# Kernel tuning notes

Hardware: AMD Instinct MI355X
Metric: run time of the kernel (lower is better)

## Reference

```python
import jax, jax.numpy as jnp
import numpy as np

NUM_ENTITIES = 100000
BATCH_SIZE = 4096
E_STATIC = 250000
E_NEW = 4096
D_ENT = 128
D_REL = 64
N_REL = 9
N_TYPES = 3
N_INTENTS = 8
NUM_LAYERS = 3
SCALE = 0.05


def _make_edges(key, n):
    ks = jax.random.split(key, 5)
    src = jax.random.randint(ks[0], (n,), 0, NUM_ENTITIES, dtype=jnp.int32)
    st = jax.random.randint(ks[1], (n,), 0, N_TYPES, dtype=jnp.int32)
    tgt = jax.random.randint(ks[2], (n,), 0, NUM_ENTITIES, dtype=jnp.int32)
    tt = jax.random.randint(ks[3], (n,), 0, N_TYPES, dtype=jnp.int32)
    rel = jax.random.randint(ks[4], (n,), 0, N_REL, dtype=jnp.int32)
    return jnp.stack([src, st, tgt, tt, rel], axis=1)


def setup_inputs() -> dict:
    key = jax.random.key(0)
    ks = jax.random.split(key, 16)
    return {
        'new_edges': _make_edges(ks[0], E_NEW),
        'new_node_types': jax.random.randint(ks[1], (BATCH_SIZE,), 0, N_TYPES, dtype=jnp.int32),
        'static_edges': _make_edges(ks[2], E_STATIC),
        'entity_embeddings': SCALE * jax.random.normal(ks[3], (NUM_ENTITIES - BATCH_SIZE, D_ENT), jnp.float32),
        'default_emb': SCALE * jax.random.normal(ks[4], (N_TYPES, D_ENT), jnp.float32),
        'relation_emb': SCALE * jax.random.normal(ks[5], (N_REL, D_REL), jnp.float32),
        'W_rel': SCALE * jax.random.normal(ks[6], (N_REL, D_ENT, D_REL), jnp.float32),
        'b_rel': SCALE * jax.random.normal(ks[7], (N_REL, D_REL), jnp.float32),
        'W_msg': SCALE * jax.random.normal(ks[8], (N_REL, D_ENT, D_ENT), jnp.float32),
        'W_intent': SCALE * jax.random.normal(ks[9], (N_TYPES, D_ENT, N_INTENTS), jnp.float32),
        'b_intent': SCALE * jax.random.normal(ks[10], (N_TYPES, N_INTENTS), jnp.float32),
        'W_ibn': SCALE * jax.random.normal(ks[11], (N_TYPES, N_INTENTS, N_REL), jnp.float32),
        'b_ibn': SCALE * jax.random.normal(ks[12], (N_TYPES, N_REL), jnp.float32),
    }


def multi_dense(lookups, values, W, b=None, act=None):
    # Same math as tf.gather(W, lookups) followed by values @ w, but computed
    # against all D (<=9) weight slices then selected, to avoid materializing
    # a [E, d_in, d_out] gathered-weights tensor.
    out_all = jnp.einsum('ei,dio->edo', values, W)  # [E, D, d_out]
    out = jnp.take_along_axis(out_all, lookups[:, None, None], axis=1)[:, 0]
    if b is not None:
        out = out + b[lookups]
    return act(out) if act is not None else out


def reference(new_edges, new_node_types, static_edges, entity_embeddings,
              default_emb, relation_emb, W_rel, b_rel, W_msg,
              W_intent, b_intent, W_ibn, b_ibn):
    edges = jnp.concatenate([new_edges, static_edges], axis=0)  # [E, 5]
    sources = edges[:, 0]
    targets = edges[:, 2]
    target_types = edges[:, 3]
    relations = edges[:, 4]

    rel_e = relation_emb[relations]  # [E, D_REL]
    # first BATCH_SIZE entity slots come from type default embeddings
    ent = jnp.concatenate([default_emb[new_node_types], entity_embeddings], axis=0)  # [N, D_ENT]

    layer_edge_weights = []
    for _ in range(NUM_LAYERS):
        src = ent[sources]  # [E, D_ENT]
        tgt = ent[targets]  # [E, D_ENT]
        # per-target intent distribution and per-relation intent weights
        intents = multi_dense(target_types, tgt, W_intent, b_intent, jax.nn.softmax)  # [E, N_INTENTS]
        rel_w = multi_dense(target_types, intents, W_ibn, b_ibn, jax.nn.softmax)  # [E, N_REL]
        iw = jnp.take_along_axis(rel_w, relations[:, None], axis=1)[:, 0]  # [E]
        # per-relation transform of source embeddings
        src_rel = multi_dense(relations, src, W_rel, b_rel, jax.nn.selu)  # [E, D_REL]
        scores = jnp.einsum('er,er,e->e', src_rel, rel_e, iw)  # [E]
        exp_s = jnp.exp(scores)
        denom = jax.ops.segment_sum(exp_s, targets, num_segments=NUM_ENTITIES)  # [N]
        # tf.math.reciprocal_no_nan semantics
        safe = jnp.where(denom != 0, denom, 1.0)
        recip = jnp.where(denom != 0, 1.0 / safe, 0.0)
        dist = exp_s * recip[targets]  # scatter-softmax over incoming edges
        # inference: dropout is identity
        msg = dist[:, None] * multi_dense(relations, src, W_msg, None, None)  # [E, D_ENT]
        ent = jax.ops.segment_sum(msg, targets, num_segments=NUM_ENTITIES)  # [N, D_ENT]
        layer_edge_weights.append(dist)

    return ent, jnp.stack(layer_edge_weights)  # [N, D_ENT], [L, E]
```

## Files before the change

### kernel.cpp

```cpp
#include <hip/hip_runtime.h>
#include <cstddef>
#include <cstdint>

#define NE 100000
#define EN 4096
#define ET 254096
#define D 128
#define DR 64
#define NR 9
#define NT 3
#define NI 8
#define TE 256
#define TILES_X 28

using frag  = __attribute__((ext_vector_type(8))) short;
using f32x4 = __attribute__((ext_vector_type(4))) float;

__device__ __forceinline__ ushort f2b(float x) {
  union { float f; uint32_t u; } v; v.f = x;
  uint32_t r = v.u + 0x7FFFu + ((v.u >> 16) & 1u);
  return (ushort)(r >> 16);
}

__device__ __forceinline__ uint32_t cvtpk(float lo, float hi) {
  uint32_t r;
  asm("v_cvt_pk_bf16_f32 %0, %1, %2" : "=v"(r) : "v"(lo), "v"(hi));
  return r;
}

__device__ __forceinline__ frag lds_rd(const ushort* b, int row, int k) {
  const int ch = ((k >> 3) ^ (row & 7));
  return *(const frag*)(b + row * D + (ch << 3));
}
__device__ __forceinline__ void lds_wr(ushort* b, int row, int ch, frag v) {
  *(frag*)(b + row * D + ((ch ^ (row & 7)) << 3)) = v;
}
__device__ __forceinline__ void lds_wr2(ushort* b, int row, int k, uint32_t v) {
  const int ch = (k >> 3) ^ (row & 7);
  *(uint32_t*)(b + row * D + (ch << 3) + (k & 7)) = v;
}

__global__ void fill_zero(float4* __restrict__ p, int n4) {
  int i = blockIdx.x * blockDim.x + threadIdx.x;
  if (i < n4) p[i] = make_float4(0.f, 0.f, 0.f, 0.f);
}

__global__ void k_init(ushort* __restrict__ entb, const int* __restrict__ ntypes,
                       const float* __restrict__ def, const float* __restrict__ emb) {
  int i = blockIdx.x * blockDim.x + threadIdx.x;
  if (i >= NE * (D / 4)) return;
  int row = i >> 5, ch = i & 31;
  float4 v;
  if (row < EN) v = ((const float4*)(def + ntypes[row] * D))[ch];
  else v = ((const float4*)(emb + (size_t)(row - EN) * D))[ch];
  ushort4 h;
  h.x = f2b(v.x); h.y = f2b(v.y); h.z = f2b(v.z); h.w = f2b(v.w);
  ((ushort4*)entb)[i] = h;
}

__global__ void k_zero_cnt(int* cnt) { if (threadIdx.x < 48) cnt[threadIdx.x] = 0; }

__global__ __launch_bounds__(256) void k_hist(const int* __restrict__ nedg,
                                              const int* __restrict__ sedg,
                                              int* __restrict__ cnt) {
  __shared__ int h[NR];
  if (threadIdx.x < NR) h[threadIdx.x] = 0;
  __syncthreads();
  int e = blockIdx.x * 256 + threadIdx.x;
  if (e < ET) {
    const int* p = (e < EN) ? nedg + (size_t)e * 5 : sedg + (size_t)(e - EN) * 5;
    atomicAdd(&h[p[4]], 1);
  }
  __syncthreads();
  if (threadIdx.x < NR && h[threadIdx.x]) atomicAdd(&cnt[threadIdx.x], h[threadIdx.x]);
}

__global__ void k_prefix(const int* __restrict__ cnt, int* __restrict__ base,
                         int* __restrict__ head) {
  if (threadIdx.x == 0) {
    int acc = 0;
    for (int r = 0; r < NR; r++) { base[r] = acc; head[r] = acc; acc += cnt[r]; }
  }
}

__global__ __launch_bounds__(256) void k_scatter2(const int* __restrict__ nedg,
                                                  const int* __restrict__ sedg,
                                                  int* __restrict__ head,
                                                  int* __restrict__ bucket) {
  __shared__ int h[NR], bb[NR];
  if (threadIdx.x < NR) h[threadIdx.x] = 0;
  __syncthreads();
  int e = blockIdx.x * 256 + threadIdx.x;
  int r = -1, pos = 0;
  if (e < ET) {
    const int* p = (e < EN) ? nedg + (size_t)e * 5 : sedg + (size_t)(e - EN) * 5;
    r = p[4];
    pos = atomicAdd(&h[r], 1);
  }
  __syncthreads();
  if (threadIdx.x < NR)
    bb[threadIdx.x] = h[threadIdx.x] ? atomicAdd(&head[threadIdx.x], h[threadIdx.x]) : 0;
  __syncthreads();
  if (r >= 0) bucket[bb[r] + pos] = e;
}

__global__ __launch_bounds__(256) void k_thist(const int* __restrict__ nedg,
                                               const int* __restrict__ sedg,
                                               int* __restrict__ thist) {
  int e = blockIdx.x * 256 + threadIdx.x;
  if (e >= ET) return;
  const int* p = (e < EN) ? nedg + (size_t)e * 5 : sedg + (size_t)(e - EN) * 5;
  atomicAdd(&thist[p[2]], 1);
}

__global__ __launch_bounds__(256) void k_scan1(const int* __restrict__ hist,
                                               int* __restrict__ local_ex,
                                               int* __restrict__ bsum, int n) {
  __shared__ int s[256];
  int i = blockIdx.x * 256 + threadIdx.x;
  int v = (i < n) ? hist[i] : 0;
  s[threadIdx.x] = v;
  __syncthreads();
  for (int off = 1; off < 256; off <<= 1) {
    int t = (threadIdx.x >= off) ? s[threadIdx.x - off] : 0;
    __syncthreads();
    s[threadIdx.x] += t;
    __syncthreads();
  }
  if (i < n) local_ex[i] = s[threadIdx.x] - v;
  if (threadIdx.x == 255) bsum[blockIdx.x] = s[255];
}

__global__ __launch_bounds__(512) void k_scan2(int* __restrict__ bsum, int nb) {
  __shared__ int s[512];
  int v = (threadIdx.x < nb) ? bsum[threadIdx.x] : 0;
  s[threadIdx.x] = v;
  __syncthreads();
  for (int off = 1; off < 512; off <<= 1) {
    int t = (threadIdx.x >= off) ? s[threadIdx.x - off] : 0;
    __syncthreads();
    s[threadIdx.x] += t;
    __syncthreads();
  }
  if (threadIdx.x < nb) bsum[threadIdx.x] = s[threadIdx.x] - v;
}

__global__ void k_scan3(int* __restrict__ tgt_off, const int* __restrict__ bsum,
                        int* __restrict__ thead) {
  int i = blockIdx.x * 256 + threadIdx.x;
  if (i < NE) {
    int v = tgt_off[i] + bsum[i >> 8];
    tgt_off[i] = v;
    thead[i] = v;
  }
  if (i == 0) tgt_off[NE] = ET;
}

__global__ __launch_bounds__(256) void k_tscatter(const int* __restrict__ nedg,
                                                  const int* __restrict__ sedg,
                                                  int* __restrict__ thead,
                                                  int* __restrict__ tpos,
                                                  int* __restrict__ esorted) {
  int e = blockIdx.x * 256 + threadIdx.x;
  if (e >= ET) return;
  const int* p = (e < EN) ? nedg + (size_t)e * 5 : sedg + (size_t)(e - EN) * 5;
  int pos = atomicAdd(&thead[p[2]], 1);
  tpos[e] = pos;
  esorted[pos] = e;
}

__global__ __launch_bounds__(256) void k_iw(
    const ushort* __restrict__ entb,
    const float* __restrict__ W_int, const float* __restrict__ b_int,
    const float* __restrict__ W_ibn, const float* __restrict__ b_ibn,
    float* __restrict__ IW) {
  __shared__ ushort sE[TE * D];
  __shared__ ushort sWi[NT * 16 * D];
  __shared__ float sInt3[TE * 25];
  __shared__ float sbint[NT * NI], sWibn[NT * NI * NR], sbibn[NT * NR];

  const int tid = threadIdx.x;
  const int lane = tid & 63, wv = tid >> 6, g = lane >> 4, c = lane & 15;

  for (int i = tid; i < NT * NI * (D / 2); i += 256) {
    int tt = i / (NI * D / 2), rem = i % (NI * D / 2), j = rem / (D / 2), k2 = rem % (D / 2);
    const float* Wi = W_int + (size_t)tt * D * NI;
    lds_wr2(sWi, tt * 16 + j, 2 * k2, cvtpk(Wi[(2 * k2) * NI + j], Wi[(2 * k2 + 1) * NI + j]));
  }
  for (int i = tid; i < NT * 8 * (D / 2); i += 256) {
    int tt = i / (8 * D / 2), rem = i % (8 * D / 2), j = rem / (D / 2), k2 = rem % (D / 2);
    lds_wr2(sWi, tt * 16 + 8 + j, 2 * k2, 0u);
  }
  for (int i = tid; i < NT * NI; i += 256) sbint[i] = b_int[i];
  for (int i = tid; i < NT * NI * NR; i += 256) sWibn[i] = W_ibn[i];
  for (int i = tid; i < NT * NR; i += 256) sbibn[i] = b_ibn[i];

  const int ebase = blockIdx.x * TE;
  for (int i = tid; i < TE * 16; i += 256) {
    int row = i >> 4, ch = i & 15;
    int ent = ebase + row;
    frag v = {};
    if (ent < NE) v = ((const frag*)(entb + (size_t)ent * D))[ch];
    lds_wr(sE, row, ch, v);
  }
  __syncthreads();

  f32x4 accI[4][NT];
#pragma unroll
  for (int mt = 0; mt < 4; mt++)
#pragma unroll
    for (int tt = 0; tt < NT; tt++) accI[mt][tt] = (f32x4){0.f, 0.f, 0.f, 0.f};
#pragma unroll
  for (int ks = 0; ks < 4; ks++) {
    const int k = ks * 32 + g * 8;
    frag b[NT];
#pragma unroll
    for (int tt = 0; tt < NT; tt++) b[tt] = lds_rd(sWi, tt * 16 + c, k);
#pragma unroll
    for (int mt = 0; mt < 4; mt++) {
      frag a = lds_rd(sE, (wv * 4 + mt) * 16 + c, k);
#pragma unroll
      for (int tt = 0; tt < NT; tt++)
        accI[mt][tt] = __builtin_amdgcn_mfma_f32_16x16x32_bf16(a, b[tt], accI[mt][tt], 0, 0, 0);
    }
  }
  if (c < NI) {
#pragma unroll
    for (int mt = 0; mt < 4; mt++) {
      const int rb = (wv * 4 + mt) * 16 + g * 4;
#pragma unroll
      for (int tt = 0; tt < NT; tt++)
#pragma unroll
        for (int q = 0; q < 4; q++) sInt3[(rb + q) * 25 + tt * 8 + c] = accI[mt][tt][q];
    }
  }
  __syncthreads();

  const int ent = ebase + tid;
  if (ent < NE) {
    float* outp = IW + (size_t)ent * NT * NR;
#pragma unroll
    for (int tt = 0; tt < NT; tt++) {
      float it[NI], mx = -1e30f;
#pragma unroll
      for (int j = 0; j < NI; j++) {
        it[j] = sInt3[tid * 25 + tt * 8 + j] + sbint[tt * NI + j];
        mx = fmaxf(mx, it[j]);
      }
      float ssum = 0.f;
#pragma unroll
      for (int j = 0; j < NI; j++) { it[j] = __expf(it[j] - mx); ssum += it[j]; }
      const float inv = 1.f / ssum;
      float qv[NR];
#pragma unroll
      for (int k = 0; k < NR; k++) qv[k] = sbibn[tt * NR + k];
#pragma unroll
      for (int j = 0; j < NI; j++) {
        const float ij = it[j] * inv;
#pragma unroll
        for (int k = 0; k < NR; k++) qv[k] = fmaf(ij, sWibn[(tt * NI + j) * NR + k], qv[k]);
      }
      float m9 = qv[0];
#pragma unroll
      for (int k = 1; k < NR; k++) m9 = fmaxf(m9, qv[k]);
      float s9 = 0.f;
#pragma unroll
      for (int k = 0; k < NR; k++) s9 += __expf(qv[k] - m9);
      const float i9 = 1.f / s9;
#pragma unroll
      for (int k = 0; k < NR; k++) outp[tt * NR + k] = __expf(qv[k] - m9) * i9;
    }
  }
}

__global__ __launch_bounds__(1024) void k_pass1(
    const ushort* __restrict__ entb,
    const int* __restrict__ nedg, const int* __restrict__ sedg,
    const int* __restrict__ cnt, const int* __restrict__ base_g,
    const int* __restrict__ bucket, const int* __restrict__ tpos,
    const float* __restrict__ IW,
    const float* __restrict__ rel_emb,
    const float* __restrict__ W_rel, const float* __restrict__ b_rel,
    const float* __restrict__ W_msg,
    ushort* __restrict__ msgbuf, float* __restrict__ exps_s) {
  const int r = blockIdx.y;
  __shared__ ushort sA[TE * D];
  __shared__ ushort sWm[D * D];
  __shared__ ushort sWr[DR * D];
  __shared__ int sTP[TE];
  __shared__ float sIW[TE];
  __shared__ float sbrel[DR], srele[DR];

  const int tid = threadIdx.x;
  const int lane = tid & 63;
  const int wv = tid >> 6;
  const int g = lane >> 4;
  const int c = lane & 15;

  const float* Wr = W_rel + (size_t)r * D * DR;
  for (int i = tid; i < (D / 2) * DR; i += 1024) {
    int k2 = i / DR, n = i % DR;
    lds_wr2(sWr, n, 2 * k2, cvtpk(Wr[(2 * k2) * DR + n], Wr[(2 * k2 + 1) * DR + n]));
  }
  const float* Wm = W_msg + (size_t)r * D * D;
  for (int i = tid; i < (D / 2) * D; i += 1024) {
    int k2 = i >> 7, n = i & 127;
    lds_wr2(sWm, n, 2 * k2, cvtpk(Wm[(2 * k2) * D + n], Wm[(2 * k2 + 1) * D + n]));
  }
  if (tid < DR) { sbrel[tid] = b_rel[r * DR + tid]; srele[tid] = rel_emb[r * DR + tid]; }

  const int nr = cnt[r];
  const int bbase = base_g[r];
  const int ntiles = (nr + TE - 1) / TE;

  for (int tile = blockIdx.x; tile < ntiles; tile += gridDim.x) {
    const int e0 = tile * TE;
    const int ne = min(TE, nr - e0);
    __syncthreads();

    {
      const int row = tid & 255, h = tid >> 8;
      int eg = 0;
      if (row < ne) eg = bucket[bbase + e0 + row];
      const int* p = (eg < EN) ? nedg + (size_t)eg * 5 : sedg + (size_t)(eg - EN) * 5;
      const int s = p[0];
      if (h == 0 && row < ne) {
        const int t = p[2], tt = p[3];
        sTP[row] = tpos[eg];
        sIW[row] = IW[((size_t)t * NT + tt) * NR + r];
      }
      const frag* rp = (const frag*)(entb + (size_t)s * D);
#pragma unroll
      for (int j = 0; j < 4; j++) lds_wr(sA, row, h * 4 + j, rp[h * 4 + j]);
    }
    __syncthreads();

    f32x4 accR[4], accM[8];
#pragma unroll
    for (int nt = 0; nt < 4; nt++) accR[nt] = (f32x4){0.f, 0.f, 0.f, 0.f};
#pragma unroll
    for (int nt = 0; nt < 8; nt++) accM[nt] = (f32x4){0.f, 0.f, 0.f, 0.f};
#pragma unroll
    for (int ks = 0; ks < 4; ks++) {
      const int k = ks * 32 + g * 8;
      frag a0 = lds_rd(sA, wv * 16 + c, k);
#pragma unroll
      for (int nt = 0; nt < 4; nt++) {
        frag b = lds_rd(sWr, nt * 16 + c, k);
        accR[nt] = __builtin_amdgcn_mfma_f32_16x16x32_bf16(a0, b, accR[nt], 0, 0, 0);
      }
#pragma unroll
      for (int nt = 0; nt < 8; nt++) {
        frag b = lds_rd(sWm, nt * 16 + c, k);
        accM[nt] = __builtin_amdgcn_mfma_f32_16x16x32_bf16(a0, b, accM[nt], 0, 0, 0);
      }
    }

    const int mb = wv * 16 + g * 4;

    float es[4];
    {
      float v[4] = {0.f, 0.f, 0.f, 0.f};
#pragma unroll
      for (int nt = 0; nt < 4; nt++) {
        const int col = nt * 16 + c;
        const float br = sbrel[col], re = srele[col];
#pragma unroll
        for (int q = 0; q < 4; q++) {
          const float x = accR[nt][q] + br;
          const float sl = x > 0.f ? 1.0507009873554805f * x
                                   : 1.7580993408473766f * (__expf(x) - 1.f);
          v[q] = fmaf(sl, re, v[q]);
        }
      }
#pragma unroll
      for (int off = 1; off < 16; off <<= 1)
#pragma unroll
        for (int q = 0; q < 4; q++) v[q] += __shfl_xor(v[q], off, 64);
#pragma unroll
      for (int q = 0; q < 4; q++) {
        const int m = mb + q;
        es[q] = __expf(v[q] * sIW[m]);
        if (c == 0 && m < ne) exps_s[sTP[m]] = es[q];
      }
    }

    {
#pragma unroll
      for (int q = 0; q < 4; q++) {
        const int m = mb + q;
        ushort* mrow = msgbuf + (size_t)sTP[m] * D;
#pragma unroll
        for (int nt = 0; nt < 8; nt++) {
          float val = accM[nt][q] * es[q];
          float other = __shfl_xor(val, 1, 64);
          if (!(c & 1) && m < ne)
            *(uint32_t*)(mrow + nt * 16 + c) = cvtpk(val, other);
        }
      }
    }
  }
}

__global__ __launch_bounds__(256) void k_agg(
    const ushort* __restrict__ msgbuf, const float* __restrict__ exps_s,
    const int* __restrict__ tgt_off, const int* __restrict__ esorted,
    ushort* __restrict__ entb, float* __restrict__ fout,
    float* __restrict__ dout, int last) {
  const int lg = threadIdx.x & 15;
  const int grp = threadIdx.x >> 4;
  const int ngrp = gridDim.x * 16;
  for (int t = blockIdx.x * 16 + grp; t < NE; t += ngrp) {
    const int beg = tgt_off[t], end = tgt_off[t + 1];
    float a[8] = {0.f, 0.f, 0.f, 0.f, 0.f, 0.f, 0.f, 0.f};
    float dsum = 0.f;
    for (int j = beg; j < end; j++) {
      const uint4 pk = *(const uint4*)(msgbuf + (size_t)j * D + lg * 8);
      dsum += exps_s[j];
      a[0] += __uint_as_float(pk.x << 16); a[1] += __uint_as_float(pk.x & 0xFFFF0000u);
      a[2] += __uint_as_float(pk.y << 16); a[3] += __uint_as_float(pk.y & 0xFFFF0000u);
      a[4] += __uint_as_float(pk.z << 16); a[5] += __uint_as_float(pk.z & 0xFFFF0000u);
      a[6] += __uint_as_float(pk.w << 16); a[7] += __uint_as_float(pk.w & 0xFFFF0000u);
    }
    const float rec = (dsum != 0.f) ? 1.f / dsum : 0.f;
#pragma unroll
    for (int i = 0; i < 8; i++) a[i] *= rec;
    if (last) {
      float4* o = (float4*)(fout + (size_t)t * D + lg * 8);
      o[0] = make_float4(a[0], a[1], a[2], a[3]);
      o[1] = make_float4(a[4], a[5], a[6], a[7]);
    } else {
      uint4 pk;
      pk.x = (uint32_t)f2b(a[0]) | ((uint32_t)f2b(a[1]) << 16);
      pk.y = (uint32_t)f2b(a[2]) | ((uint32_t)f2b(a[3]) << 16);
      pk.z = (uint32_t)f2b(a[4]) | ((uint32_t)f2b(a[5]) << 16);
      pk.w = (uint32_t)f2b(a[6]) | ((uint32_t)f2b(a[7]) << 16);
      *(uint4*)(entb + (size_t)t * D + lg * 8) = pk;
    }
    for (int j = beg + lg; j < end; j += 16) dout[esorted[j]] = exps_s[j] * rec;
  }
}

extern "C" void kernel_launch(void* const* d_in, const int* in_sizes, int n_in,
                              void* d_out, int out_size, void* d_ws, size_t ws_size,
                              hipStream_t stream) {
  const int* nedg = (const int*)d_in[0];
  const int* ntypes = (const int*)d_in[1];
  const int* sedg = (const int*)d_in[2];
  const float* emb = (const float*)d_in[3];
  const float* def = (const float*)d_in[4];
  const float* rel_emb = (const float*)d_in[5];
  const float* W_rel = (const float*)d_in[6];
  const float* b_rel = (const float*)d_in[7];
  const float* W_msg = (const float*)d_in[8];
  const float* W_int = (const float*)d_in[9];
  const float* b_int = (const float*)d_in[10];
  const float* W_ibn = (const float*)d_in[11];
  const float* b_ibn = (const float*)d_in[12];
  float* out = (float*)d_out;

  char* w = (char*)d_ws;
  size_t off = 0;
  ushort* entb = (ushort*)(w + off); off += (size_t)NE * D * 2;
  ushort* msgbuf = (ushort*)(w + off); off += (size_t)ET * D * 2;
  float* exps_s = (float*)(w + off); off += (size_t)ET * 4;
  int* bucket = (int*)(w + off); off += (size_t)ET * 4;
  int* tpos = (int*)(w + off); off += (size_t)ET * 4;
  int* esorted = (int*)(w + off); off += (size_t)ET * 4;
  int* tgt_off = (int*)(w + off); off += (size_t)(NE + 4) * 4;
  int* thead = (int*)(w + off); off += (size_t)NE * 4;
  int* thist = (int*)(w + off); off += (size_t)NE * 4;
  int* bsum = (int*)(w + off); off += 2048;
  int* cnt = (int*)(w + off); off += 192;
  float* IW = (float*)(w + off); off += (size_t)NE * NT * NR * 4;
  int* base_g = cnt + 16;
  int* head = cnt + 32;
  float* dist_base = out + (size_t)NE * D;

  const int eblocks = (ET + 255) / 256;
  const int nb = (NE + 255) / 256;

  k_init<<<dim3((NE * (D / 4) + 255) / 256), 256, 0, stream>>>(entb, ntypes, def, emb);
  k_zero_cnt<<<1, 64, 0, stream>>>(cnt);
  k_hist<<<dim3(eblocks), 256, 0, stream>>>(nedg, sedg, cnt);
  k_prefix<<<1, 64, 0, stream>>>(cnt, base_g, head);
  k_scatter2<<<dim3(eblocks), 256, 0, stream>>>(nedg, sedg, head, bucket);

  fill_zero<<<dim3((NE / 4 + 255) / 256), 256, 0, stream>>>((float4*)thist, NE / 4);
  k_thist<<<dim3(eblocks), 256, 0, stream>>>(nedg, sedg, thist);
  k_scan1<<<dim3(nb), 256, 0, stream>>>(thist, tgt_off, bsum, NE);
  k_scan2<<<1, 512, 0, stream>>>(bsum, nb);
  k_scan3<<<dim3(nb), 256, 0, stream>>>(tgt_off, bsum, thead);
  k_tscatter<<<dim3(eblocks), 256, 0, stream>>>(nedg, sedg, thead, tpos, esorted);

  for (int l = 0; l < 3; l++) {
    k_iw<<<dim3(nb), 256, 0, stream>>>(entb, W_int, b_int, W_ibn, b_ibn, IW);
    k_pass1<<<dim3(TILES_X, NR), 1024, 0, stream>>>(
        entb, nedg, sedg, cnt, base_g, bucket, tpos, IW, rel_emb, W_rel, b_rel, W_msg,
        msgbuf, exps_s);
    k_agg<<<dim3(2048), 256, 0, stream>>>(msgbuf, exps_s, tgt_off, esorted, entb, out,
                                          dist_base + (size_t)l * ET, l == 2);
  }
}
```

Before: 399.2 us.

## Fuse edge-sorting preprocessing kernels and widen k_iw to 1024 threads

Merges the relation histogram with the target histogram, and the relation bucket scatter with the target scatter, which removes several launches and repeated reads of the edge arrays. The fill_zero kernel is replaced by hipMemsetAsync. k_iw now runs 1024 threads per block with one M-tile per wave and stages its IW output through LDS so the global stores are coalesced. Weight loads in k_iw and k_pass1 are batched into registers before the bf16 convert and LDS writes, to get more loads in flight.

```diff
diff --git a/kernel.cpp b/kernel.cpp
--- a/kernel.cpp
+++ b/kernel.cpp
@@ -38,11 +38,6 @@
 __device__ __forceinline__ void lds_wr2(ushort* b, int row, int k, uint32_t v) {
   const int ch = (k >> 3) ^ (row & 7);
   *(uint32_t*)(b + row * D + (ch << 3) + (k & 7)) = v;
-}
-
-__global__ void fill_zero(float4* __restrict__ p, int n4) {
-  int i = blockIdx.x * blockDim.x + threadIdx.x;
-  if (i < n4) p[i] = make_float4(0.f, 0.f, 0.f, 0.f);
 }
 
 __global__ void k_init(ushort* __restrict__ entb, const int* __restrict__ ntypes,
@@ -60,9 +55,10 @@
 
 __global__ void k_zero_cnt(int* cnt) { if (threadIdx.x < 48) cnt[threadIdx.x] = 0; }
 
-__global__ __launch_bounds__(256) void k_hist(const int* __restrict__ nedg,
-                                              const int* __restrict__ sedg,
-                                              int* __restrict__ cnt) {
+__global__ __launch_bounds__(256) void k_hist2(const int* __restrict__ nedg,
+                                               const int* __restrict__ sedg,
+                                               int* __restrict__ cnt,
+                                               int* __restrict__ thist) {
   __shared__ int h[NR];
   if (threadIdx.x < NR) h[threadIdx.x] = 0;
   __syncthreads();
@@ -70,6 +66,7 @@
   if (e < ET) {
     const int* p = (e < EN) ? nedg + (size_t)e * 5 : sedg + (size_t)(e - EN) * 5;
     atomicAdd(&h[p[4]], 1);
+    atomicAdd(&thist[p[2]], 1);
   }
   __syncthreads();
   if (threadIdx.x < NR && h[threadIdx.x]) atomicAdd(&cnt[threadIdx.x], h[threadIdx.x]);
@@ -81,36 +78,6 @@
     int acc = 0;
     for (int r = 0; r < NR; r++) { base[r] = acc; head[r] = acc; acc += cnt[r]; }
   }
-}
-
-__global__ __launch_bounds__(256) void k_scatter2(const int* __restrict__ nedg,
-                                                  const int* __restrict__ sedg,
-                                                  int* __restrict__ head,
-                                                  int* __restrict__ bucket) {
-  __shared__ int h[NR], bb[NR];
-  if (threadIdx.x < NR) h[threadIdx.x] = 0;
-  __syncthreads();
-  int e = blockIdx.x * 256 + threadIdx.x;
-  int r = -1, pos = 0;
-  if (e < ET) {
-    const int* p = (e < EN) ? nedg + (size_t)e * 5 : sedg + (size_t)(e - EN) * 5;
-    r = p[4];
-    pos = atomicAdd(&h[r], 1);
-  }
-  __syncthreads();
-  if (threadIdx.x < NR)
-    bb[threadIdx.x] = h[threadIdx.x] ? atomicAdd(&head[threadIdx.x], h[threadIdx.x]) : 0;
-  __syncthreads();
-  if (r >= 0) bucket[bb[r] + pos] = e;
-}
-
-__global__ __launch_bounds__(256) void k_thist(const int* __restrict__ nedg,
-                                               const int* __restrict__ sedg,
-                                               int* __restrict__ thist) {
-  int e = blockIdx.x * 256 + threadIdx.x;
-  if (e >= ET) return;
-  const int* p = (e < EN) ? nedg + (size_t)e * 5 : sedg + (size_t)(e - EN) * 5;
-  atomicAdd(&thist[p[2]], 1);
 }
 
 __global__ __launch_bounds__(256) void k_scan1(const int* __restrict__ hist,
@@ -156,20 +123,36 @@
   if (i == 0) tgt_off[NE] = ET;
 }
 
-__global__ __launch_bounds__(256) void k_tscatter(const int* __restrict__ nedg,
+__global__ __launch_bounds__(256) void k_scatter3(const int* __restrict__ nedg,
                                                   const int* __restrict__ sedg,
+                                                  int* __restrict__ head,
                                                   int* __restrict__ thead,
+                                                  int* __restrict__ bucket,
                                                   int* __restrict__ tpos,
                                                   int* __restrict__ esorted) {
+  __shared__ int h[NR], bb[NR];
+  if (threadIdx.x < NR) h[threadIdx.x] = 0;
+  __syncthreads();
   int e = blockIdx.x * 256 + threadIdx.x;
-  if (e >= ET) return;
-  const int* p = (e < EN) ? nedg + (size_t)e * 5 : sedg + (size_t)(e - EN) * 5;
-  int pos = atomicAdd(&thead[p[2]], 1);
-  tpos[e] = pos;
-  esorted[pos] = e;
-}
-
-__global__ __launch_bounds__(256) void k_iw(
+  int r = -1, pos = 0, t = 0;
+  if (e < ET) {
+    const int* p = (e < EN) ? nedg + (size_t)e * 5 : sedg + (size_t)(e - EN) * 5;
+    r = p[4]; t = p[2];
+    pos = atomicAdd(&h[r], 1);
+  }
+  __syncthreads();
+  if (threadIdx.x < NR)
+    bb[threadIdx.x] = h[threadIdx.x] ? atomicAdd(&head[threadIdx.x], h[threadIdx.x]) : 0;
+  __syncthreads();
+  if (r >= 0) {
+    bucket[bb[r] + pos] = e;
+    int pt = atomicAdd(&thead[t], 1);
+    tpos[e] = pt;
+    esorted[pt] = e;
+  }
+}
+
+__global__ __launch_bounds__(1024) void k_iw(
     const ushort* __restrict__ entb,
     const float* __restrict__ W_int, const float* __restrict__ b_int,
     const float* __restrict__ W_ibn, const float* __restrict__ b_ibn,
@@ -182,69 +165,83 @@
   const int tid = threadIdx.x;
   const int lane = tid & 63, wv = tid >> 6, g = lane >> 4, c = lane & 15;
 
-  for (int i = tid; i < NT * NI * (D / 2); i += 256) {
-    int tt = i / (NI * D / 2), rem = i % (NI * D / 2), j = rem / (D / 2), k2 = rem % (D / 2);
-    const float* Wi = W_int + (size_t)tt * D * NI;
-    lds_wr2(sWi, tt * 16 + j, 2 * k2, cvtpk(Wi[(2 * k2) * NI + j], Wi[(2 * k2 + 1) * NI + j]));
-  }
-  for (int i = tid; i < NT * 8 * (D / 2); i += 256) {
+  {
+    float a[2], b[2];
+#pragma unroll
+    for (int j = 0; j < 2; j++) {
+      int i = tid + j * 1024;
+      if (i < NT * NI * (D / 2)) {
+        int tt = i / (NI * D / 2), rem = i % (NI * D / 2), jj = rem / (D / 2), k2 = rem % (D / 2);
+        const float* Wi = W_int + (size_t)tt * D * NI;
+        a[j] = Wi[(2 * k2) * NI + jj]; b[j] = Wi[(2 * k2 + 1) * NI + jj];
+      }
+    }
+#pragma unroll
+    for (int j = 0; j < 2; j++) {
+      int i = tid + j * 1024;
+      if (i < NT * NI * (D / 2)) {
+        int tt = i / (NI * D / 2), rem = i % (NI * D / 2), jj = rem / (D / 2), k2 = rem % (D / 2);
+        lds_wr2(sWi, tt * 16 + jj, 2 * k2, cvtpk(a[j], b[j]));
+      }
+    }
+  }
+  for (int i = tid; i < NT * 8 * (D / 2); i += 1024) {
     int tt = i / (8 * D / 2), rem = i % (8 * D / 2), j = rem / (D / 2), k2 = rem % (D / 2);
     lds_wr2(sWi, tt * 16 + 8 + j, 2 * k2, 0u);
   }
-  for (int i = tid; i < NT * NI; i += 256) sbint[i] = b_int[i];
-  for (int i = tid; i < NT * NI * NR; i += 256) sWibn[i] = W_ibn[i];
-  for (int i = tid; i < NT * NR; i += 256) sbibn[i] = b_ibn[i];
+  if (tid < NT * NI) sbint[tid] = b_int[tid];
+  for (int i = tid; i < NT * NI * NR; i += 1024) sWibn[i] = W_ibn[i];
+  if (tid < NT * NR) sbibn[tid] = b_ibn[tid];
 
   const int ebase = blockIdx.x * TE;
-  for (int i = tid; i < TE * 16; i += 256) {
-    int row = i >> 4, ch = i & 15;
-    int ent = ebase + row;
-    frag v = {};
-    if (ent < NE) v = ((const frag*)(entb + (size_t)ent * D))[ch];
-    lds_wr(sE, row, ch, v);
-  }
-  __syncthreads();
-
-  f32x4 accI[4][NT];
-#pragma unroll
-  for (int mt = 0; mt < 4; mt++)
-#pragma unroll
-    for (int tt = 0; tt < NT; tt++) accI[mt][tt] = (f32x4){0.f, 0.f, 0.f, 0.f};
-#pragma unroll
-  for (int ks = 0; ks < 4; ks++) {
-    const int k = ks * 32 + g * 8;
-    frag b[NT];
-#pragma unroll
-    for (int tt = 0; tt < NT; tt++) b[tt] = lds_rd(sWi, tt * 16 + c, k);
-#pragma unroll
-    for (int mt = 0; mt < 4; mt++) {
-      frag a = lds_rd(sE, (wv * 4 + mt) * 16 + c, k);
+  const int nrow = min(TE, NE - ebase);
+  {
+    frag tmp[4];
+#pragma unroll
+    for (int j = 0; j < 4; j++) {
+      int i = tid + j * 1024, row = i >> 4, ch = i & 15;
+      tmp[j] = (row < nrow) ? ((const frag*)(entb + (size_t)(ebase + row) * D))[ch] : (frag){};
+    }
+#pragma unroll
+    for (int j = 0; j < 4; j++) {
+      int i = tid + j * 1024, row = i >> 4, ch = i & 15;
+      lds_wr(sE, row, ch, tmp[j]);
+    }
+  }
+  __syncthreads();
+
+  {
+    f32x4 accI[NT];
+#pragma unroll
+    for (int tt = 0; tt < NT; tt++) accI[tt] = (f32x4){0.f, 0.f, 0.f, 0.f};
+#pragma unroll
+    for (int ks = 0; ks < 4; ks++) {
+      const int k = ks * 32 + g * 8;
+      frag a = lds_rd(sE, wv * 16 + c, k);
+#pragma unroll
+      for (int tt = 0; tt < NT; tt++) {
+        frag b = lds_rd(sWi, tt * 16 + c, k);
+        accI[tt] = __builtin_amdgcn_mfma_f32_16x16x32_bf16(a, b, accI[tt], 0, 0, 0);
+      }
+    }
+    if (c < NI) {
+      const int rb = wv * 16 + g * 4;
 #pragma unroll
       for (int tt = 0; tt < NT; tt++)
-        accI[mt][tt] = __builtin_amdgcn_mfma_f32_16x16x32_bf16(a, b[tt], accI[mt][tt], 0, 0, 0);
-    }
-  }
-  if (c < NI) {
-#pragma unroll
-    for (int mt = 0; mt < 4; mt++) {
-      const int rb = (wv * 4 + mt) * 16 + g * 4;
-#pragma unroll
-      for (int tt = 0; tt < NT; tt++)
-#pragma unroll
-        for (int q = 0; q < 4; q++) sInt3[(rb + q) * 25 + tt * 8 + c] = accI[mt][tt][q];
-    }
-  }
-  __syncthreads();
-
-  const int ent = ebase + tid;
-  if (ent < NE) {
-    float* outp = IW + (size_t)ent * NT * NR;
-#pragma unroll
-    for (int tt = 0; tt < NT; tt++) {
+#pragma unroll
+        for (int q = 0; q < 4; q++) sInt3[(rb + q) * 25 + tt * 8 + c] = accI[tt][q];
+    }
+  }
+  __syncthreads();
+
+  float* stg = (float*)sE;
+  {
+    const int row = tid & 255, tt = tid >> 8;
+    if (tt < NT && row < nrow) {
       float it[NI], mx = -1e30f;
 #pragma unroll
       for (int j = 0; j < NI; j++) {
-        it[j] = sInt3[tid * 25 + tt * 8 + j] + sbint[tt * NI + j];
+        it[j] = sInt3[row * 25 + tt * 8 + j] + sbint[tt * NI + j];
         mx = fmaxf(mx, it[j]);
       }
       float ssum = 0.f;
@@ -268,9 +265,14 @@
       for (int k = 0; k < NR; k++) s9 += __expf(qv[k] - m9);
       const float i9 = 1.f / s9;
 #pragma unroll
-      for (int k = 0; k < NR; k++) outp[tt * NR + k] = __expf(qv[k] - m9) * i9;
-    }
-  }
+      for (int k = 0; k < NR; k++) stg[row * 27 + tt * 9 + k] = __expf(qv[k] - m9) * i9;
+    }
+  }
+  __syncthreads();
+
+  const int n27 = nrow * 27;
+  float* outp = IW + (size_t)ebase * 27;
+  for (int i = tid; i < n27; i += 1024) outp[i] = stg[i];
 }
 
 __global__ __launch_bounds__(1024) void k_pass1(
@@ -297,15 +299,30 @@
   const int g = lane >> 4;
   const int c = lane & 15;
 
-  const float* Wr = W_rel + (size_t)r * D * DR;
-  for (int i = tid; i < (D / 2) * DR; i += 1024) {
-    int k2 = i / DR, n = i % DR;
-    lds_wr2(sWr, n, 2 * k2, cvtpk(Wr[(2 * k2) * DR + n], Wr[(2 * k2 + 1) * DR + n]));
-  }
-  const float* Wm = W_msg + (size_t)r * D * D;
-  for (int i = tid; i < (D / 2) * D; i += 1024) {
-    int k2 = i >> 7, n = i & 127;
-    lds_wr2(sWm, n, 2 * k2, cvtpk(Wm[(2 * k2) * D + n], Wm[(2 * k2 + 1) * D + n]));
+  {
+    const float* Wr = W_rel + (size_t)r * D * DR;
+    const float* Wm = W_msg + (size_t)r * D * D;
+    float ra[4], rb[4], ma[8], mb[8];
+#pragma unroll
+    for (int j = 0; j < 4; j++) {
+      int i = tid + j * 1024, k2 = i / DR, n = i % DR;
+      ra[j] = Wr[(2 * k2) * DR + n]; rb[j] = Wr[(2 * k2 + 1) * DR + n];
+    }
+#pragma unroll
+    for (int j = 0; j < 8; j++) {
+      int i = tid + j * 1024, k2 = i >> 7, n = i & 127;
+      ma[j] = Wm[(2 * k2) * D + n]; mb[j] = Wm[(2 * k2 + 1) * D + n];
+    }
+#pragma unroll
+    for (int j = 0; j < 4; j++) {
+      int i = tid + j * 1024, k2 = i / DR, n = i % DR;
+      lds_wr2(sWr, n, 2 * k2, cvtpk(ra[j], rb[j]));
+    }
+#pragma unroll
+    for (int j = 0; j < 8; j++) {
+      int i = tid + j * 1024, k2 = i >> 7, n = i & 127;
+      lds_wr2(sWm, n, 2 * k2, cvtpk(ma[j], mb[j]));
+    }
   }
   if (tid < DR) { sbrel[tid] = b_rel[r * DR + tid]; srele[tid] = rel_emb[r * DR + tid]; }
 
@@ -330,8 +347,11 @@
         sIW[row] = IW[((size_t)t * NT + tt) * NR + r];
       }
       const frag* rp = (const frag*)(entb + (size_t)s * D);
-#pragma unroll
-      for (int j = 0; j < 4; j++) lds_wr(sA, row, h * 4 + j, rp[h * 4 + j]);
+      frag tmp[4];
+#pragma unroll
+      for (int j = 0; j < 4; j++) tmp[j] = rp[h * 4 + j];
+#pragma unroll
+      for (int j = 0; j < 4; j++) lds_wr(sA, row, h * 4 + j, tmp[j]);
     }
     __syncthreads();
 
@@ -482,19 +502,17 @@
 
   k_init<<<dim3((NE * (D / 4) + 255) / 256), 256, 0, stream>>>(entb, ntypes, def, emb);
   k_zero_cnt<<<1, 64, 0, stream>>>(cnt);
-  k_hist<<<dim3(eblocks), 256, 0, stream>>>(nedg, sedg, cnt);
+  hipMemsetAsync(thist, 0, (size_t)NE * 4, stream);
+  k_hist2<<<dim3(eblocks), 256, 0, stream>>>(nedg, sedg, cnt, thist);
   k_prefix<<<1, 64, 0, stream>>>(cnt, base_g, head);
-  k_scatter2<<<dim3(eblocks), 256, 0, stream>>>(nedg, sedg, head, bucket);
-
-  fill_zero<<<dim3((NE / 4 + 255) / 256), 256, 0, stream>>>((float4*)thist, NE / 4);
-  k_thist<<<dim3(eblocks), 256, 0, stream>>>(nedg, sedg, thist);
   k_scan1<<<dim3(nb), 256, 0, stream>>>(thist, tgt_off, bsum, NE);
   k_scan2<<<1, 512, 0, stream>>>(bsum, nb);
   k_scan3<<<dim3(nb), 256, 0, stream>>>(tgt_off, bsum, thead);
-  k_tscatter<<<dim3(eblocks), 256, 0, stream>>>(nedg, sedg, thead, tpos, esorted);
+  k_scatter3<<<dim3(eblocks), 256, 0, stream>>>(nedg, sedg, head, thead, bucket, tpos,
+                                                esorted);
 
   for (int l = 0; l < 3; l++) {
-    k_iw<<<dim3(nb), 256, 0, stream>>>(entb, W_int, b_int, W_ibn, b_ibn, IW);
+    k_iw<<<dim3(nb), 1024, 0, stream>>>(entb, W_int, b_int, W_ibn, b_ibn, IW);
     k_pass1<<<dim3(TILES_X, NR), 1024, 0, stream>>>(
         entb, nedg, sedg, cnt, base_g, bucket, tpos, IW, rel_emb, W_rel, b_rel, W_msg,
         msgbuf, exps_s);
```

New measurement: 357.1 us. 10.6% less time.
